# Kernel tuning notes

Hardware: AMD Instinct MI355X
Metric: run time of the kernel (lower is better)

Reference implementation:

```python
import jax, jax.numpy as jnp
import numpy as np

N_HEADS, N_LEVELS, N_POINTS = 8, 4, 4
D_MODEL, UNIT = 384, 128

@jax.custom_vjp
def grl(x):
    # Gradient Reversal Layer: identity forward, -grad backward (lambda_=1)
    return x

def _grl_fwd(x):
    return x, None

def _grl_bwd(res, g):
    return (-g,)

grl.defvjp(_grl_fwd, _grl_bwd)


def ms_deform_attn_core(value, spatial_shapes_np, loc, attn):
    """Multi-scale deformable attention (grid_sample bilinear, zeros padding, align_corners=False).
    value: (N, Len_in, nH, hd)   loc: (N, Lq, nH, nL, nP, 2) normalized [0,1]   attn: (N, Lq, nH, nL, nP)
    """
    N, Lq, nH, nL, nP, _ = loc.shape
    hd = value.shape[-1]
    b = jnp.arange(N).reshape(N, 1, 1, 1)
    h = jnp.arange(nH).reshape(1, 1, nH, 1)
    out = jnp.zeros((N, Lq, nH, hd), dtype=value.dtype)
    start = 0
    for l in range(nL):
        H, W = int(spatial_shapes_np[l, 0]), int(spatial_shapes_np[l, 1])
        v = value[:, start:start + H * W]  # (N, H*W, nH, hd)
        start += H * W
        # align_corners=False pixel coords
        x = loc[:, :, :, l, :, 0] * W - 0.5
        y = loc[:, :, :, l, :, 1] * H - 0.5
        x0f, y0f = jnp.floor(x), jnp.floor(y)
        lx, ly = x - x0f, y - y0f
        x0, y0 = x0f.astype(jnp.int32), y0f.astype(jnp.int32)
        def gather(xi, yi):
            valid = ((xi >= 0) & (xi < W) & (yi >= 0) & (yi < H)).astype(value.dtype)
            flat = jnp.clip(yi, 0, H - 1) * W + jnp.clip(xi, 0, W - 1)  # (N,Lq,nH,nP)
            return v[b, flat, h] * valid[..., None]  # (N,Lq,nH,nP,hd)
        s = (((1 - lx) * (1 - ly))[..., None] * gather(x0, y0)
             + (lx * (1 - ly))[..., None] * gather(x0 + 1, y0)
             + ((1 - lx) * ly)[..., None] * gather(x0, y0 + 1)
             + (lx * ly)[..., None] * gather(x0 + 1, y0 + 1))
        out = out + jnp.sum(s * attn[:, :, :, l, :, None], axis=3)
    return out.reshape(N, Lq, nH * hd)


def setup_inputs() -> dict:
    key = jax.random.key(0)
    ks = jax.random.split(key, 12)
    N, Lq = 2, 5440
    spatial = np.array([[64, 64], [32, 32], [16, 16], [8, 8]], dtype=np.int32)
    sizes = spatial[:, 0] * spatial[:, 1]
    Len_in = int(sizes.sum())  # 5440
    lsi = np.concatenate([[0], np.cumsum(sizes)[:-1]]).astype(np.int32)
    D, U, nH, nL, nP = D_MODEL, UNIT, N_HEADS, N_LEVELS, N_POINTS
    def lin(k, fin, fout):
        return jax.random.normal(k, (fin, fout), jnp.float32) / np.sqrt(fin)
    # faithful grid-init bias for sampling offsets
    thetas = np.arange(nH) * (2.0 * np.pi / nH)
    grid = np.stack([np.cos(thetas), np.sin(thetas)], -1)
    grid = grid / np.abs(grid).max(-1, keepdims=True)
    grid = np.tile(grid.reshape(nH, 1, 1, 2), (1, nL, nP, 1))
    for i in range(nP):
        grid[:, :, i, :] *= (i + 1)
    return {
        "query": jax.random.normal(ks[0], (N, Lq, D), jnp.float32),
        "reference_points": jax.random.uniform(ks[1], (N, Lq, nL, 2), jnp.float32),
        "input_flatten": jax.random.normal(ks[2], (N, Len_in, D), jnp.float32),
        "input_spatial_shapes": jnp.asarray(spatial),
        "input_level_start_index": jnp.asarray(lsi),
        "W_off": 0.01 * jax.random.normal(ks[3], (2 * U, nH * nL * nP * 2), jnp.float32),
        "b_off": jnp.asarray(grid.reshape(-1), dtype=jnp.float32),
        "W_attn": lin(ks[4], 2 * U, nH * nL * nP),
        "b_attn": jnp.zeros((nH * nL * nP,), jnp.float32),
        "W_val": lin(ks[5], 2 * U, 3 * U),
        "b_val": jnp.zeros((3 * U,), jnp.float32),
        "W_out": lin(ks[6], 3 * U, 2 * U),
        "b_out": jnp.zeros((2 * U,), jnp.float32),
        "W_attn_zd": lin(ks[7], 3 * U, nH * nL * nP),
        "b_attn_zd": jnp.zeros((nH * nL * nP,), jnp.float32),
        "W_val_zd": lin(ks[8], D, D),
        "b_val_zd": jnp.zeros((D,), jnp.float32),
        "W_out_zd": lin(ks[9], D, U),
        "b_out_zd": jnp.zeros((U,), jnp.float32),
    }


def reference(query, reference_points, input_flatten, input_spatial_shapes, input_level_start_index,
              W_off, b_off, W_attn, b_attn, W_val, b_val, W_out, b_out,
              W_attn_zd, b_attn_zd, W_val_zd, b_val_zd, W_out_zd, b_out_zd):
    N, Lq, _ = query.shape
    nH, nL, nP, U = N_HEADS, N_LEVELS, N_POINTS, UNIT
    ss = np.asarray(input_spatial_shapes)  # static level shapes
    sample_query = query[..., :2 * U]
    off = (sample_query @ W_off + b_off).reshape(N, Lq, nH, nL, nP, 2)
    # offset normalizer = [W_l, H_l] per level
    norm = jnp.asarray(np.stack([ss[:, 1], ss[:, 0]], -1), dtype=query.dtype)
    loc = reference_points[:, :, None, :, None, :] + off / norm[None, None, None, :, None, :]
    # top (content) path
    top_val = (input_flatten[..., :2 * U] @ W_val + b_val).reshape(N, -1, nH, 3 * U // nH)
    aw = jax.nn.softmax((sample_query @ W_attn + b_attn).reshape(N, Lq, nH, nL * nP), -1)
    aw = aw.reshape(N, Lq, nH, nL, nP)
    top_out = ms_deform_attn_core(top_val, ss, loc, aw) @ W_out + b_out
    # bottom (domain) path with gradient reversal on content slice
    bot_val_in = jnp.concatenate([grl(input_flatten[..., :2 * U]), input_flatten[..., 2 * U:]], -1)
    bot_val = (bot_val_in @ W_val_zd + b_val_zd).reshape(N, -1, nH, D_MODEL // nH)
    bot_query = jnp.concatenate([grl(query[..., :2 * U]), query[..., 2 * U:]], -1)
    aw_zd = jax.nn.softmax((bot_query @ W_attn_zd + b_attn_zd).reshape(N, Lq, nH, nL * nP), -1)
    aw_zd = aw_zd.reshape(N, Lq, nH, nL, nP)
    bot_out = ms_deform_attn_core(bot_val, ss, loc, aw_zd) @ W_out_zd + b_out_zd
    return jnp.concatenate([top_out, bot_out], -1)
```

## Files before the change

### kernel.cpp

```cpp
#include <hip/hip_runtime.h>
#include <hip/hip_bf16.h>
#include <math.h>

#define DM   384
#define U2   256
#define HD   48

typedef __attribute__((ext_vector_type(8))) short short8;
typedef __attribute__((ext_vector_type(4))) float floatx4;

static __device__ __forceinline__ unsigned short f2bfbits(float f) {
    __hip_bfloat16 h = __float2bfloat16(f);
    return *reinterpret_cast<unsigned short*>(&h);
}
static __device__ __forceinline__ unsigned pack2(float x, float y) {
    return (unsigned)f2bfbits(x) | ((unsigned)f2bfbits(y) << 16);
}
static __device__ __forceinline__ float bflo(unsigned u) { return __uint_as_float(u << 16); }
static __device__ __forceinline__ float bfhi(unsigned u) { return __uint_as_float(u & 0xffff0000u); }

struct PrepParams {
    const float* wsrc[7]; __hip_bfloat16* wdst[7];
    int K[7], N[7], off[8];
    int total;
};
__global__ __launch_bounds__(256) void prep_kernel(PrepParams d) {
    const int iw = blockIdx.x * 256 + threadIdx.x;
    if (iw >= d.total) return;
    int s = 0;
#pragma unroll
    for (int i = 1; i < 7; ++i) if (iw >= d.off[i]) s = i;
    const int r = iw - d.off[s];
    const int k = r / d.N[s], n = r - k * d.N[s];
    d.wdst[s][(size_t)n * d.K[s] + k] = __float2bfloat16(d.wsrc[s][r]);
}

struct Seg {
    const void* A; int lda; int aty;
    const __hip_bfloat16* Bt; int ldbt;
    const float* bias; void* C; int ldc; int K; int omode;
};
struct SegParams { Seg seg[5]; int ystart[5]; int nseg; };

__global__ __launch_bounds__(256) void gemm_seg_kernel(SegParams p) {
    __shared__ __hip_bfloat16 As[64 * 40];
    __shared__ __hip_bfloat16 Bs[64 * 40];

    const int yb = blockIdx.y;
    int s = 0;
#pragma unroll
    for (int i = 1; i < 5; ++i) if (i < p.nseg && yb >= p.ystart[i]) s = i;
    Seg sg;
    switch (s) {
        case 0: sg = p.seg[0]; break;
        case 1: sg = p.seg[1]; break;
        case 2: sg = p.seg[2]; break;
        case 3: sg = p.seg[3]; break;
        default: sg = p.seg[4]; break;
    }
    const int by = yb - p.ystart[s];

    const int t    = threadIdx.x;
    const int bm   = blockIdx.x * 64;
    const int bn   = by * 64;
    const int w    = t >> 6, lane = t & 63;
    const int wm   = (w >> 1) * 32, wn = (w & 1) * 32;
    const int quad = lane >> 4, lm = lane & 15;

    const int r0 = t >> 2, kc = (t & 3) * 8;

    float4 fa0, fa1;
    short8 abf;
    short8 bbf;

    const bool atyb = (sg.aty != 0);

#define LOAD_REGS(K0)                                                          \
    do {                                                                       \
        if (atyb) {                                                            \
            abf = *(const short8*)((const __hip_bfloat16*)sg.A +               \
                (size_t)(bm + r0) * sg.lda + (K0) + kc);                       \
        } else {                                                               \
            const float* _src = (const float*)sg.A +                           \
                (size_t)(bm + r0) * sg.lda + (K0) + kc;                        \
            fa0 = *(const float4*)_src;                                        \
            fa1 = *(const float4*)(_src + 4);                                  \
        }                                                                      \
        bbf = *(const short8*)&sg.Bt[(size_t)(bn + r0) * sg.ldbt + (K0) + kc]; \
    } while (0)

    floatx4 acc[2][2] = {};

    LOAD_REGS(0);
    for (int k0 = 0; k0 < sg.K; k0 += 32) {
        if (atyb) {
            *(short8*)&As[r0 * 40 + kc] = abf;
        } else {
            uint4 u;
            u.x = pack2(fa0.x, fa0.y); u.y = pack2(fa0.z, fa0.w);
            u.z = pack2(fa1.x, fa1.y); u.w = pack2(fa1.z, fa1.w);
            *(uint4*)&As[r0 * 40 + kc] = u;
        }
        *(short8*)&Bs[r0 * 40 + kc] = bbf;
        __syncthreads();

        const int kn = k0 + 32;
        if (kn < sg.K) LOAD_REGS(kn);

        short8 af[2], bf[2];
#pragma unroll
        for (int i = 0; i < 2; ++i)
            af[i] = *(const short8*)&As[(wm + i * 16 + lm) * 40 + quad * 8];
#pragma unroll
        for (int j = 0; j < 2; ++j)
            bf[j] = *(const short8*)&Bs[(wn + j * 16 + lm) * 40 + quad * 8];
#pragma unroll
        for (int i = 0; i < 2; ++i)
#pragma unroll
            for (int j = 0; j < 2; ++j)
                acc[i][j] = __builtin_amdgcn_mfma_f32_16x16x32_bf16(
                    af[i], bf[j], acc[i][j], 0, 0, 0);
        __syncthreads();
    }
#undef LOAD_REGS

#pragma unroll
    for (int i = 0; i < 2; ++i)
#pragma unroll
        for (int reg = 0; reg < 4; ++reg) {
            const int row = bm + wm + i * 16 + quad * 4 + reg;
#pragma unroll
            for (int j = 0; j < 2; ++j) {
                const int col = bn + wn + j * 16 + lm;
                const float v = acc[i][j][reg] + sg.bias[col];
                if (sg.omode == 0) {
                    ((float*)sg.C)[(size_t)row * sg.ldc + col] = v;
                } else if (sg.omode == 1) {
                    ((__hip_bfloat16*)sg.C)[(size_t)row * sg.ldc + col] = __float2bfloat16(v);
                } else {
                    const int h = col / 48;
                    const size_t idx = (size_t)row * 768 + h * 96 +
                                       ((sg.omode == 3) ? 48 : 0) + (col - h * 48);
                    ((__hip_bfloat16*)sg.C)[idx] = __float2bfloat16(v);
                }
            }
        }
}

#define SPP 524

__global__ __launch_bounds__(192) void sampler_kernel(
    const float* __restrict__ off_buf,
    const float* __restrict__ logit_top,
    const float* __restrict__ logit_bot,
    const float* __restrict__ ref_pts,
    const int*   __restrict__ ss,
    const int*   __restrict__ lsi,
    const __hip_bfloat16* __restrict__ vcomb,
    __hip_bfloat16* __restrict__ core_top,
    __hip_bfloat16* __restrict__ core_bot,
    int Lq, int LenIn)
{
    __shared__ float    sA[2][128];
    __shared__ unsigned sP[2][SPP];
    __shared__ float4   sRed[96][2];

    const int bid = blockIdx.x;
    const int t   = threadIdx.x;

    float gw[4];
    int   gp[4];

    if (t < 128) {
        const int e = t;
        const int l = (e >> 2) & 3;
        const float2 offv = *(const float2*)&off_buf[(size_t)bid * 256 + 2 * e];
        const float rx = ref_pts[(size_t)(bid * 4 + l) * 2 + 0];
        const float ry = ref_pts[(size_t)(bid * 4 + l) * 2 + 1];
        const int H = ss[2 * l], W = ss[2 * l + 1];
        const int start = lsi[l];

        const float x = (rx + offv.x / (float)W) * (float)W - 0.5f;
        const float y = (ry + offv.y / (float)H) * (float)H - 0.5f;
        const float x0f = floorf(x), y0f = floorf(y);
        const float lx = x - x0f, ly = y - y0f;
        const int ix0 = (int)x0f, iy0 = (int)y0f;
        const int ix1 = ix0 + 1,  iy1 = iy0 + 1;

        const float vx0 = (ix0 >= 0 && ix0 < W) ? 1.f : 0.f;
        const float vx1 = (ix1 >= 0 && ix1 < W) ? 1.f : 0.f;
        const float vy0 = (iy0 >= 0 && iy0 < H) ? 1.f : 0.f;
        const float vy1 = (iy1 >= 0 && iy1 < H) ? 1.f : 0.f;
        const int cx0 = min(max(ix0, 0), W - 1);
        const int cx1 = min(max(ix1, 0), W - 1);
        const int cy0 = min(max(iy0, 0), H - 1);
        const int cy1 = min(max(iy1, 0), H - 1);
        const int base = bid / Lq * LenIn + start;

        gp[0] = base + cy0 * W + cx0;
        gp[1] = base + cy0 * W + cx1;
        gp[2] = base + cy1 * W + cx0;
        gp[3] = base + cy1 * W + cx1;
        gw[0] = (1.f - lx) * (1.f - ly) * vx0 * vy0;
        gw[1] = lx * (1.f - ly) * vx1 * vy0;
        gw[2] = (1.f - lx) * ly * vx0 * vy1;
        gw[3] = lx * ly * vx1 * vy1;
    }

    if (t < 16) {
        const int br = t >> 3;
        const int h  = t & 7;
        const float* L = (br ? logit_bot : logit_top) + (size_t)bid * 128 + h * 16;
        float lg[16];
        *(float4*)&lg[0]  = *(const float4*)&L[0];
        *(float4*)&lg[4]  = *(const float4*)&L[4];
        *(float4*)&lg[8]  = *(const float4*)&L[8];
        *(float4*)&lg[12] = *(const float4*)&L[12];
        float m = -1e30f;
#pragma unroll
        for (int j = 0; j < 16; ++j) m = fmaxf(m, lg[j]);
        float ex[16], sum = 0.f;
#pragma unroll
        for (int j = 0; j < 16; ++j) { ex[j] = expf(lg[j] - m); sum += ex[j]; }
        const float inv = 1.f / sum;
#pragma unroll
        for (int j = 0; j < 16; ++j) sA[br][h * 16 + j] = ex[j] * inv;
    }
    __syncthreads();

    if (t < 128) {
        const int e = t;
        const int pidx = 4 * e + (e >> 4);
#pragma unroll
        for (int br = 0; br < 2; ++br) {
            const float a = sA[br][e];
#pragma unroll
            for (int k = 0; k < 4; ++k) {
                sP[br][pidx + k] =
                    ((unsigned)f2bfbits(gw[k] * a) << 16) | (unsigned)gp[k];
            }
        }
    }
    __syncthreads();

    const int half = t / 96;
    const int u    = t - half * 96;
    const int g    = u / 6;
    const int m    = u - g * 6;
    const int br   = g & 1;
    const int h    = g >> 1;

    const unsigned* P = sP[br];
    const char* vb = (const char*)vcomb + h * 192 + br * 96 + m * 16;

    float a0 = 0.f, a1 = 0.f, a2 = 0.f, a3 = 0.f;
    float a4 = 0.f, a5 = 0.f, a6 = 0.f, a7 = 0.f;
    const int lp0 = half * 8;
#pragma unroll
    for (int lp = 0; lp < 8; ++lp) {
        const int ib = 65 * h + 4 * (lp0 + lp);
#pragma unroll
        for (int k = 0; k < 4; ++k) {
            const unsigned uu = P[ib + k];
            const float wv = __uint_as_float(uu & 0xffff0000u);
            const unsigned pt = uu & 0x3fffu;
            const uint4 v = *(const uint4*)(vb + pt * 1536u);
            a0 = fmaf(wv, bflo(v.x), a0);
            a1 = fmaf(wv, bfhi(v.x), a1);
            a2 = fmaf(wv, bflo(v.y), a2);
            a3 = fmaf(wv, bfhi(v.y), a3);
            a4 = fmaf(wv, bflo(v.z), a4);
            a5 = fmaf(wv, bfhi(v.z), a5);
            a6 = fmaf(wv, bflo(v.w), a6);
            a7 = fmaf(wv, bfhi(v.w), a7);
        }
    }

    if (half) {
        float4 p0; p0.x = a0; p0.y = a1; p0.z = a2; p0.w = a3;
        float4 p1; p1.x = a4; p1.y = a5; p1.z = a6; p1.w = a7;
        sRed[u][0] = p0;
        sRed[u][1] = p1;
    }
    __syncthreads();
    if (!half) {
        const float4 p0 = sRed[u][0];
        const float4 p1 = sRed[u][1];
        uint4 o;
        o.x = pack2(a0 + p0.x, a1 + p0.y);
        o.y = pack2(a2 + p0.z, a3 + p0.w);
        o.z = pack2(a4 + p1.x, a5 + p1.y);
        o.w = pack2(a6 + p1.z, a7 + p1.w);
        __hip_bfloat16* dst = br ? core_bot : core_top;
        *(uint4*)&dst[(size_t)bid * DM + h * HD + m * 8] = o;
    }
}

extern "C" void kernel_launch(void* const* d_in, const int* in_sizes, int n_in,
                              void* d_out, int out_size, void* d_ws, size_t ws_size,
                              hipStream_t stream) {
    const float* query   = (const float*)d_in[0];
    const float* refpts  = (const float*)d_in[1];
    const float* flat    = (const float*)d_in[2];
    const int*   ss      = (const int*)d_in[3];
    const int*   lsi     = (const int*)d_in[4];
    const float* W_off   = (const float*)d_in[5];
    const float* b_off   = (const float*)d_in[6];
    const float* W_attn  = (const float*)d_in[7];
    const float* b_attn  = (const float*)d_in[8];
    const float* W_val   = (const float*)d_in[9];
    const float* b_val   = (const float*)d_in[10];
    const float* W_out   = (const float*)d_in[11];
    const float* b_out   = (const float*)d_in[12];
    const float* W_attn_zd = (const float*)d_in[13];
    const float* b_attn_zd = (const float*)d_in[14];
    const float* W_val_zd  = (const float*)d_in[15];
    const float* b_val_zd  = (const float*)d_in[16];
    const float* W_out_zd  = (const float*)d_in[17];
    const float* b_out_zd  = (const float*)d_in[18];

    const int Lq    = in_sizes[0] / (2 * DM);
    const int LenIn = in_sizes[2] / (2 * DM);
    const int M  = 2 * Lq;
    const int Mv = 2 * LenIn;

    float* out = (float*)d_out;

    float* ws      = (float*)d_ws;
    float* off_buf = ws;
    float* lt      = off_buf + (size_t)M * 256;
    float* lb      = lt + (size_t)M * 128;
    __hip_bfloat16* vcomb = (__hip_bfloat16*)(lb + (size_t)M * 128);
    __hip_bfloat16* ct    = vcomb + (size_t)Mv * 768;
    __hip_bfloat16* cb    = ct + (size_t)M * 384;
    __hip_bfloat16* wtb   = cb + (size_t)M * 384;

    PrepParams pp;
    const float* srcs[7] = {W_attn, W_attn_zd, W_val, W_val_zd, W_out, W_out_zd, W_off};
    const int Ks[7] = {256, 384, 256, 384, 384, 384, 256};
    const int Ns[7] = {128, 128, 384, 384, 256, 128, 256};
    __hip_bfloat16* dsts[7];
    int off = 0;
    for (int i = 0; i < 7; ++i) {
        pp.wsrc[i] = srcs[i]; pp.K[i] = Ks[i]; pp.N[i] = Ns[i];
        pp.off[i] = off;
        dsts[i] = wtb + off;
        pp.wdst[i] = dsts[i];
        off += Ks[i] * Ns[i];
    }
    pp.off[7] = off;
    pp.total = off;

    const dim3 blk(256);
    const int mg = M / 64;

    prep_kernel<<<dim3((pp.total + 255) / 256), blk, 0, stream>>>(pp);

    {
        SegParams p;
        p.seg[0] = { query, DM, 0, dsts[6], 256, b_off,     off_buf, 256, 256, 0 };
        p.seg[1] = { query, DM, 0, dsts[0], 256, b_attn,    lt,      128, 256, 0 };
        p.seg[2] = { query, DM, 0, dsts[1], 384, b_attn_zd, lb,      128, 384, 0 };
        p.seg[3] = { flat,  DM, 0, dsts[2], 256, b_val,     vcomb,   0,   256, 2 };
        p.seg[4] = { flat,  DM, 0, dsts[3], 384, b_val_zd,  vcomb,   0,   384, 3 };
        p.ystart[0] = 0; p.ystart[1] = 4; p.ystart[2] = 6;
        p.ystart[3] = 8; p.ystart[4] = 14;
        p.nseg = 5;
        gemm_seg_kernel<<<dim3(mg, 20), blk, 0, stream>>>(p);
    }

    sampler_kernel<<<dim3(M), dim3(192), 0, stream>>>(
        off_buf, lt, lb, refpts, ss, lsi, vcomb, ct, cb, Lq, LenIn);

    {
        SegParams p;
        p.seg[0] = { ct, DM, 1, dsts[4], 384, b_out,    out,      DM, 384, 0 };
        p.seg[1] = { cb, DM, 1, dsts[5], 384, b_out_zd, out + U2, DM, 384, 0 };
        p.ystart[0] = 0; p.ystart[1] = 4;
        p.nseg = 2;
        gemm_seg_kernel<<<dim3(mg, 6), blk, 0, stream>>>(p);
    }
}
```

Baseline: 229.9 us.

## Pre-convert query and input activations to bf16 and pack sampler FMAs

The prep kernel now also converts the fp32 query and input_flatten tensors to bf16 buffers in the workspace. The fused GEMM therefore loads only bf16 A tiles, dropping the per-tile fp32 load and pack path and the runtime type branch. Each fp32 activation is otherwise re-read and re-converted by every N-tile block of the segmented GEMM. Separately, the sampler accumulation is rewritten with float2 vectors so the compiler can emit packed FMA instructions, and the gather address is computed with a single 32-bit offset. The cost is an extra pass that writes and re-reads the bf16 activation copies, plus added workspace.

```diff
diff --git a/kernel.cpp b/kernel.cpp
--- a/kernel.cpp
+++ b/kernel.cpp
@@ -8,6 +8,7 @@
 
 typedef __attribute__((ext_vector_type(8))) short short8;
 typedef __attribute__((ext_vector_type(4))) float floatx4;
+typedef __attribute__((ext_vector_type(2))) float floatx2;
 
 static __device__ __forceinline__ unsigned short f2bfbits(float f) {
     __hip_bfloat16 h = __float2bfloat16(f);
@@ -20,13 +21,30 @@
 static __device__ __forceinline__ float bfhi(unsigned u) { return __uint_as_float(u & 0xffff0000u); }
 
 struct PrepParams {
+    const float* q; const float* f;
+    __hip_bfloat16 *q_bf, *f_bf;
     const float* wsrc[7]; __hip_bfloat16* wdst[7];
     int K[7], N[7], off[8];
-    int total;
+    int nQ4, nF4, total;
 };
 __global__ __launch_bounds__(256) void prep_kernel(PrepParams d) {
-    const int iw = blockIdx.x * 256 + threadIdx.x;
-    if (iw >= d.total) return;
+    const int idx = blockIdx.x * 256 + threadIdx.x;
+    if (idx >= d.total) return;
+    if (idx < d.nQ4) {
+        const int i4 = idx * 4;
+        const float4 v = *(const float4*)&d.q[i4];
+        uint2 pk; pk.x = pack2(v.x, v.y); pk.y = pack2(v.z, v.w);
+        *(uint2*)&d.q_bf[i4] = pk;
+        return;
+    }
+    if (idx < d.nQ4 + d.nF4) {
+        const int i4 = (idx - d.nQ4) * 4;
+        const float4 v = *(const float4*)&d.f[i4];
+        uint2 pk; pk.x = pack2(v.x, v.y); pk.y = pack2(v.z, v.w);
+        *(uint2*)&d.f_bf[i4] = pk;
+        return;
+    }
+    const int iw = idx - d.nQ4 - d.nF4;
     int s = 0;
 #pragma unroll
     for (int i = 1; i < 7; ++i) if (iw >= d.off[i]) s = i;
@@ -36,7 +54,7 @@
 }
 
 struct Seg {
-    const void* A; int lda; int aty;
+    const __hip_bfloat16* A; int lda;
     const __hip_bfloat16* Bt; int ldbt;
     const float* bias; void* C; int ldc; int K; int omode;
 };
@@ -69,43 +87,24 @@
 
     const int r0 = t >> 2, kc = (t & 3) * 8;
 
-    float4 fa0, fa1;
-    short8 abf;
-    short8 bbf;
-
-    const bool atyb = (sg.aty != 0);
-
-#define LOAD_REGS(K0)                                                          \
-    do {                                                                       \
-        if (atyb) {                                                            \
-            abf = *(const short8*)((const __hip_bfloat16*)sg.A +               \
-                (size_t)(bm + r0) * sg.lda + (K0) + kc);                       \
-        } else {                                                               \
-            const float* _src = (const float*)sg.A +                           \
-                (size_t)(bm + r0) * sg.lda + (K0) + kc;                        \
-            fa0 = *(const float4*)_src;                                        \
-            fa1 = *(const float4*)(_src + 4);                                  \
-        }                                                                      \
-        bbf = *(const short8*)&sg.Bt[(size_t)(bn + r0) * sg.ldbt + (K0) + kc]; \
-    } while (0)
+    const __hip_bfloat16* Ap = sg.A  + (size_t)(bm + r0) * sg.lda  + kc;
+    const __hip_bfloat16* Bp = sg.Bt + (size_t)(bn + r0) * sg.ldbt + kc;
+
+    short8 abf = *(const short8*)Ap;
+    short8 bbf = *(const short8*)Bp;
 
     floatx4 acc[2][2] = {};
 
-    LOAD_REGS(0);
     for (int k0 = 0; k0 < sg.K; k0 += 32) {
-        if (atyb) {
-            *(short8*)&As[r0 * 40 + kc] = abf;
-        } else {
-            uint4 u;
-            u.x = pack2(fa0.x, fa0.y); u.y = pack2(fa0.z, fa0.w);
-            u.z = pack2(fa1.x, fa1.y); u.w = pack2(fa1.z, fa1.w);
-            *(uint4*)&As[r0 * 40 + kc] = u;
-        }
+        *(short8*)&As[r0 * 40 + kc] = abf;
         *(short8*)&Bs[r0 * 40 + kc] = bbf;
         __syncthreads();
 
         const int kn = k0 + 32;
-        if (kn < sg.K) LOAD_REGS(kn);
+        if (kn < sg.K) {
+            abf = *(const short8*)(Ap + kn);
+            bbf = *(const short8*)(Bp + kn);
+        }
 
         short8 af[2], bf[2];
 #pragma unroll
@@ -122,7 +121,6 @@
                     af[i], bf[j], acc[i][j], 0, 0, 0);
         __syncthreads();
     }
-#undef LOAD_REGS
 
 #pragma unroll
     for (int i = 0; i < 2; ++i)
@@ -251,10 +249,11 @@
     const int h    = g >> 1;
 
     const unsigned* P = sP[br];
-    const char* vb = (const char*)vcomb + h * 192 + br * 96 + m * 16;
-
-    float a0 = 0.f, a1 = 0.f, a2 = 0.f, a3 = 0.f;
-    float a4 = 0.f, a5 = 0.f, a6 = 0.f, a7 = 0.f;
+    const char* vbase = (const char*)vcomb;
+    const unsigned tco = (unsigned)(h * 192 + br * 96 + m * 16);
+
+    floatx2 ac0 = {0.f, 0.f}, ac1 = {0.f, 0.f};
+    floatx2 ac2 = {0.f, 0.f}, ac3 = {0.f, 0.f};
     const int lp0 = half * 8;
 #pragma unroll
     for (int lp = 0; lp < 8; ++lp) {
@@ -263,22 +262,23 @@
         for (int k = 0; k < 4; ++k) {
             const unsigned uu = P[ib + k];
             const float wv = __uint_as_float(uu & 0xffff0000u);
-            const unsigned pt = uu & 0x3fffu;
-            const uint4 v = *(const uint4*)(vb + pt * 1536u);
-            a0 = fmaf(wv, bflo(v.x), a0);
-            a1 = fmaf(wv, bfhi(v.x), a1);
-            a2 = fmaf(wv, bflo(v.y), a2);
-            a3 = fmaf(wv, bfhi(v.y), a3);
-            a4 = fmaf(wv, bflo(v.z), a4);
-            a5 = fmaf(wv, bfhi(v.z), a5);
-            a6 = fmaf(wv, bflo(v.w), a6);
-            a7 = fmaf(wv, bfhi(v.w), a7);
+            const unsigned off = (uu & 0x3fffu) * 1536u + tco;
+            const uint4 v = *(const uint4*)(vbase + off);
+            floatx2 wv2 = {wv, wv};
+            floatx2 f0 = {bflo(v.x), bfhi(v.x)};
+            floatx2 f1 = {bflo(v.y), bfhi(v.y)};
+            floatx2 f2 = {bflo(v.z), bfhi(v.z)};
+            floatx2 f3 = {bflo(v.w), bfhi(v.w)};
+            ac0 += wv2 * f0;
+            ac1 += wv2 * f1;
+            ac2 += wv2 * f2;
+            ac3 += wv2 * f3;
         }
     }
 
     if (half) {
-        float4 p0; p0.x = a0; p0.y = a1; p0.z = a2; p0.w = a3;
-        float4 p1; p1.x = a4; p1.y = a5; p1.z = a6; p1.w = a7;
+        float4 p0; p0.x = ac0.x; p0.y = ac0.y; p0.z = ac1.x; p0.w = ac1.y;
+        float4 p1; p1.x = ac2.x; p1.y = ac2.y; p1.z = ac3.x; p1.w = ac3.y;
         sRed[u][0] = p0;
         sRed[u][1] = p1;
     }
@@ -287,10 +287,10 @@
         const float4 p0 = sRed[u][0];
         const float4 p1 = sRed[u][1];
         uint4 o;
-        o.x = pack2(a0 + p0.x, a1 + p0.y);
-        o.y = pack2(a2 + p0.z, a3 + p0.w);
-        o.z = pack2(a4 + p1.x, a5 + p1.y);
-        o.w = pack2(a6 + p1.z, a7 + p1.w);
+        o.x = pack2(ac0.x + p0.x, ac0.y + p0.y);
+        o.y = pack2(ac1.x + p0.z, ac1.y + p0.w);
+        o.z = pack2(ac2.x + p1.x, ac2.y + p1.y);
+        o.w = pack2(ac3.x + p1.z, ac3.y + p1.w);
         __hip_bfloat16* dst = br ? core_bot : core_top;
         *(uint4*)&dst[(size_t)bid * DM + h * HD + m * 8] = o;
     }
@@ -330,12 +330,16 @@
     float* off_buf = ws;
     float* lt      = off_buf + (size_t)M * 256;
     float* lb      = lt + (size_t)M * 128;
-    __hip_bfloat16* vcomb = (__hip_bfloat16*)(lb + (size_t)M * 128);
+    __hip_bfloat16* q_bf  = (__hip_bfloat16*)(lb + (size_t)M * 128);
+    __hip_bfloat16* f_bf  = q_bf + (size_t)M * 384;
+    __hip_bfloat16* vcomb = f_bf + (size_t)Mv * 384;
     __hip_bfloat16* ct    = vcomb + (size_t)Mv * 768;
     __hip_bfloat16* cb    = ct + (size_t)M * 384;
     __hip_bfloat16* wtb   = cb + (size_t)M * 384;
 
     PrepParams pp;
+    pp.q = query; pp.f = flat;
+    pp.q_bf = q_bf; pp.f_bf = f_bf;
     const float* srcs[7] = {W_attn, W_attn_zd, W_val, W_val_zd, W_out, W_out_zd, W_off};
     const int Ks[7] = {256, 384, 256, 384, 384, 384, 256};
     const int Ns[7] = {128, 128, 384, 384, 256, 128, 256};
@@ -349,7 +353,9 @@
         off += Ks[i] * Ns[i];
     }
     pp.off[7] = off;
-    pp.total = off;
+    pp.nQ4 = M * DM / 4;
+    pp.nF4 = Mv * DM / 4;
+    pp.total = pp.nQ4 + pp.nF4 + off;
 
     const dim3 blk(256);
     const int mg = M / 64;
@@ -358,11 +364,11 @@
 
     {
         SegParams p;
-        p.seg[0] = { query, DM, 0, dsts[6], 256, b_off,     off_buf, 256, 256, 0 };
-        p.seg[1] = { query, DM, 0, dsts[0], 256, b_attn,    lt,      128, 256, 0 };
-        p.seg[2] = { query, DM, 0, dsts[1], 384, b_attn_zd, lb,      128, 384, 0 };
-        p.seg[3] = { flat,  DM, 0, dsts[2], 256, b_val,     vcomb,   0,   256, 2 };
-        p.seg[4] = { flat,  DM, 0, dsts[3], 384, b_val_zd,  vcomb,   0,   384, 3 };
+        p.seg[0] = { q_bf, DM, dsts[6], 256, b_off,     off_buf, 256, 256, 0 };
+        p.seg[1] = { q_bf, DM, dsts[0], 256, b_attn,    lt,      128, 256, 0 };
+        p.seg[2] = { q_bf, DM, dsts[1], 384, b_attn_zd, lb,      128, 384, 0 };
+        p.seg[3] = { f_bf, DM, dsts[2], 256, b_val,     vcomb,   0,   256, 2 };
+        p.seg[4] = { f_bf, DM, dsts[3], 384, b_val_zd,  vcomb,   0,   384, 3 };
         p.ystart[0] = 0; p.ystart[1] = 4; p.ystart[2] = 6;
         p.ystart[3] = 8; p.ystart[4] = 14;
         p.nseg = 5;
@@ -374,8 +380,8 @@
 
     {
         SegParams p;
-        p.seg[0] = { ct, DM, 1, dsts[4], 384, b_out,    out,      DM, 384, 0 };
-        p.seg[1] = { cb, DM, 1, dsts[5], 384, b_out_zd, out + U2, DM, 384, 0 };
+        p.seg[0] = { ct, DM, dsts[4], 384, b_out,    out,      DM, 384, 0 };
+        p.seg[1] = { cb, DM, dsts[5], 384, b_out_zd, out + U2, DM, 384, 0 };
         p.ystart[0] = 0; p.ystart[1] = 4;
         p.nseg = 2;
         gemm_seg_kernel<<<dim3(mg, 6), blk, 0, stream>>>(p);
```

New measurement: 220.3 us. 4.2% less time.
